# Kernel optimization log

Hardware: AMD Instinct MI355X
Metric: run time of the kernel (lower is better)

Reference implementation:

```python
import jax, jax.numpy as jnp
import numpy as np

WINDOW = 3
RATIO = 5


def _box_filter(x, win):
    """Depthwise 3D box (mean) filter, 'same' padding, per channel.
    x: [N, C, D, H, W] -> [N, C, D, H, W]
    Matches torch conv3d with ones([1,1,w,w,w])/w^3 applied per channel.
    """
    c = x.shape[1]
    k = jnp.ones((c, 1, win, win, win), x.dtype) / (win ** 3)
    pad = win // 2
    return jax.lax.conv_general_dilated(
        x, k,
        window_strides=(1, 1, 1),
        padding=[(pad, pad)] * 3,
        dimension_numbers=('NCDHW', 'OIDHW', 'NCDHW'),
        feature_group_count=c,
    )


def setup_inputs() -> dict:
    key = jax.random.key(0)
    k1, k2 = jax.random.split(key)
    y_pred = jax.random.normal(k1, (1, 3, 192, 192, 192), dtype=jnp.float32)
    y_true = jax.random.uniform(k2, (1, 1, 192, 192, 192), dtype=jnp.float32)
    return {"y_pred": y_pred, "y_true": y_true}


def reference(y_pred, y_true):
    # Finite differences (abs), each [1, 3, D-1, H-1, W-1]
    base = y_pred[:, :, :-1, :-1, :-1]
    dy = jnp.abs(y_pred[:, :, 1:, :-1, :-1] - base)
    dx = jnp.abs(y_pred[:, :, :-1, 1:, :-1] - base)
    dz = jnp.abs(y_pred[:, :, :-1, :-1, 1:] - base)

    # 9 box-filtered single-channel maps == 3 depthwise box filters
    fx = _box_filter(dx, WINDOW)
    fy = _box_filter(dy, WINDOW)
    fz = _box_filter(dz, WINDOW)
    dxdx, dxdy, dxdz = fx[:, 1:2], fy[:, 1:2], fz[:, 1:2]
    dydx, dydy, dydz = fx[:, 0:1], fy[:, 0:1], fz[:, 0:1]
    dzdx, dzdy, dzdz = fx[:, 2:3], fy[:, 2:3], fz[:, 2:3]

    # Neo-Hookean invariants
    det_1 = (dxdx + 1) * ((dydy + 1) * (dzdz + 1) - dydz * dzdy)
    det_2 = -dxdy * (dydx * (dzdz + 1) - dydz * dzdx)
    det_3 = dxdz * (dydx * dzdy - (dydy + 1) * dzdx)
    J = det_1 + det_2 + det_3

    Tr = ((dxdx + 1) ** 2 + dxdy ** 2 + dxdz ** 2
          + dydx ** 2 + (dydy + 1) ** 2 + dydz ** 2
          + dzdx ** 2 + dzdy ** 2 + (dzdz + 1) ** 2)

    # mode == 'exp'
    stretch = Tr * jnp.exp(-J + 1) - 3
    vol_change = (J - 1) ** 2

    # Faithful replication of the sequential mu/lambda normalization in torch:
    mu = 1.0
    lam = mu * RATIO
    mu = mu / (mu + lam)          # 1/6
    lam = lam / (mu + lam)        # 30/31 (uses updated mu, as in source)

    U = mu / 2 * stretch + lam / 2 * vol_change
    return jnp.mean(U)
```

## Files before the change

kernel.cpp:

```cpp
#include <hip/hip_runtime.h>
#include <math.h>

#define DIM 192
#define OD  191
#define PLANE 36864
#define VOL  7077888
#define TH  16
#define TW  16
#define NBH 12
#define CD  14
#define NCH 14

typedef float f4 __attribute__((ext_vector_type(4)));
typedef _Float16 h8 __attribute__((ext_vector_type(8)));
typedef _Float16 h2 __attribute__((ext_vector_type(2)));

__global__ __launch_bounds__(256, 8)
void nh_fused_kernel(const float* __restrict__ P, float* __restrict__ out) {
    const int tid = threadIdx.x;
    const int tx  = tid & 15;
    const int ty  = tid >> 4;
    const int w0  = blockIdx.x * TW;
    const int h0  = blockIdx.y * TH;
    const int ds  = blockIdx.z * CD;
    const int de  = min(ds + CD, OD);

    __shared__ f4 sraw[2][19][20];
    __shared__ h8 sA[18][19];
    __shared__ h2 sB[18][19];
    __shared__ float wsum[4];

    const bool valid = (w0 + tx < OD) && (h0 + ty < OD);

    h8 a0 = (h8)0, a1 = (h8)0, a2 = (h8)0;
    h2 b0 = (h2)0, b1 = (h2)0, b2 = (h2)0;
    float acc = 0.f;

    for (int t = ds - 1; t <= de + 1; ++t) {
        const int cb = t & 1, pb = cb ^ 1;

        if (t >= 0 && t < DIM) {
            for (int l = tid; l < 19 * 19; l += 256) {
                const int hh = l / 19;
                const int ww = l - hh * 19;
                const int hp = h0 - 1 + hh;
                const int wp = w0 - 1 + ww;
                if (hp >= 0 && hp < DIM && wp >= 0 && wp < DIM) {
                    const size_t base = ((size_t)t * DIM + (size_t)hp) * DIM + (size_t)wp;
                    f4 r;
                    r.x = P[base];
                    r.y = P[base + VOL];
                    r.z = P[base + 2 * VOL];
                    r.w = 0.f;
                    sraw[cb][hh][ww] = r;
                }
            }
        }
        __syncthreads();

        const int p = t - 1;
        const bool pplane = (p >= 0) && (p < OD) && (t >= ds);
        for (int l = tid; l < 18 * 18; l += 256) {
            const int hh = l / 18;
            const int ww = l - hh * 18;
            const int hp = h0 - 1 + hh;
            const int wp = w0 - 1 + ww;
            h8 va = (h8)0;
            h2 vb = (h2)0;
            if (pplane && hp >= 0 && hp < OD && wp >= 0 && wp < OD) {
                const f4 c  = sraw[pb][hh][ww];
                const f4 ch = sraw[pb][hh + 1][ww];
                const f4 cw = sraw[pb][hh][ww + 1];
                const f4 cd = sraw[cb][hh][ww];
                const float hx = fabsf(ch.x - c.x), hy = fabsf(ch.y - c.y), hz = fabsf(ch.z - c.z);
                const float dx_ = fabsf(cd.x - c.x), dy_ = fabsf(cd.y - c.y), dz_ = fabsf(cd.z - c.z);
                const float wx = fabsf(cw.x - c.x), wy = fabsf(cw.y - c.y), wz = fabsf(cw.z - c.z);
                va = (h8){(_Float16)hx, (_Float16)hy, (_Float16)hz,
                          (_Float16)dx_, (_Float16)dy_, (_Float16)dz_,
                          (_Float16)wx, (_Float16)wy};
                vb = (h2){(_Float16)wz, (_Float16)0.f};
            }
            sA[hh][ww] = va;
            sB[hh][ww] = vb;
        }
        __syncthreads();

        a0 = a1; a1 = a2; b0 = b1; b1 = b2;
        {
            h8 sa = (h8)0;
            h2 sb = (h2)0;
            #pragma unroll
            for (int j = 0; j < 3; ++j) {
                #pragma unroll
                for (int k = 0; k < 3; ++k) {
                    sa += sA[ty + j][tx + k];
                    sb += sB[ty + j][tx + k];
                }
            }
            a2 = sa; b2 = sb;
        }

        const int d = t - 2;
        if (valid && d >= ds && d < de) {
            const h8 FA = a0 + a1 + a2;
            const h2 FB = b0 + b1 + b2;
            const float inv27 = 1.f / 27.f;
            const float dydx = (float)FA[0] * inv27, dxdx = (float)FA[1] * inv27, dzdx = (float)FA[2] * inv27;
            const float dydy = (float)FA[3] * inv27, dxdy = (float)FA[4] * inv27, dzdy = (float)FA[5] * inv27;
            const float dydz = (float)FA[6] * inv27, dxdz = (float)FA[7] * inv27, dzdz = (float)FB[0] * inv27;
            const float a = dxdx + 1.f, e = dydy + 1.f, iN = dzdz + 1.f;
            const float J = a * (e * iN - dydz * dzdy)
                          - dxdy * (dydx * iN - dydz * dzdx)
                          + dxdz * (dydx * dzdy - e * dzdx);
            const float Tr = a * a + dxdy * dxdy + dxdz * dxdz
                           + dydx * dydx + e * e + dydz * dydz
                           + dzdx * dzdx + dzdy * dzdy + iN * iN;
            const float stretch = Tr * expf(1.f - J) - 3.f;
            const float vol = (J - 1.f) * (J - 1.f);
            acc += 0.0833333358f * stretch + 0.4838709677f * vol;
        }
    }

    acc *= (1.f / 6967871.f);

    #pragma unroll
    for (int off = 32; off > 0; off >>= 1) acc += __shfl_down(acc, off, 64);
    if ((tid & 63) == 0) wsum[tid >> 6] = acc;
    __syncthreads();
    if (tid == 0) {
        atomicAdd(out, wsum[0] + wsum[1] + wsum[2] + wsum[3]);
    }
}

extern "C" void kernel_launch(void* const* d_in, const int* in_sizes, int n_in,
                              void* d_out, int out_size, void* d_ws, size_t ws_size,
                              hipStream_t stream) {
    const float* y_pred = (const float*)d_in[0];
    float* out = (float*)d_out;

    hipMemsetAsync(out, 0, sizeof(float), stream);

    dim3 grid(NBH, NBH, NCH);
    nh_fused_kernel<<<grid, 256, 0, stream>>>(y_pred, out);
}
```

Measured before the change: 190.6 us.

## Use DPP cross-lane W-sums and register-resident center plane to cut LDS traffic

Restructures the tile so each thread owns one loaded voxel kept in registers across planes. The W-direction 3-tap sum now uses DPP row shifts instead of LDS reads, and the output tile narrows to 14 columns so halos fit inside 16-lane rows. Only H-direction sums go through shared memory, and depth chunks grow to 24 planes to reduce halo reloads. The cost is a per-thread register carry, two extra wavefronts handling halo rows, narrower output tiles that waste 2 of 16 lanes, and lower occupancy bounds.

```diff
diff --git a/kernel.cpp b/kernel.cpp
--- a/kernel.cpp
+++ b/kernel.cpp
@@ -3,19 +3,54 @@
 
 #define DIM 192
 #define OD  191
-#define PLANE 36864
-#define VOL  7077888
+#define VOL 7077888
+#define TW  14
 #define TH  16
-#define TW  16
+#define CD  24
+#define NBW 14
 #define NBH 12
-#define CD  14
-#define NCH 14
-
-typedef float f4 __attribute__((ext_vector_type(4)));
+#define NCH 8
+
+typedef float    f4 __attribute__((ext_vector_type(4)));
 typedef _Float16 h8 __attribute__((ext_vector_type(8)));
 typedef _Float16 h2 __attribute__((ext_vector_type(2)));
 
-__global__ __launch_bounds__(256, 8)
+template<int CTRL>
+__device__ __forceinline__ int dppi(int x) {
+    return __builtin_amdgcn_update_dpp(0, x, CTRL, 0xF, 0xF, true);
+}
+
+union U8 { h8 v; int i[4]; };
+union U2 { h2 v; int i; };
+
+__device__ __forceinline__ void wsum3(h8& a, h2& b) {
+    U8 ua, s1, s2;
+    ua.v = a;
+    #pragma unroll
+    for (int k = 0; k < 4; ++k) {
+        s1.i[k] = dppi<0x101>(ua.i[k]);
+        s2.i[k] = dppi<0x111>(ua.i[k]);
+    }
+    a = ua.v + s1.v + s2.v;
+    U2 ub, t1, t2;
+    ub.v = b;
+    t1.i = dppi<0x101>(ub.i);
+    t2.i = dppi<0x111>(ub.i);
+    b = ub.v + t1.v + t2.v;
+}
+
+__device__ __forceinline__ void make_diff(const f4 c, const f4 cw, const f4 ch, const f4 cd,
+                                          h8& va, h2& vb) {
+    const float hx  = fabsf(ch.x - c.x), hy  = fabsf(ch.y - c.y), hz  = fabsf(ch.z - c.z);
+    const float dx_ = fabsf(cd.x - c.x), dy_ = fabsf(cd.y - c.y), dz_ = fabsf(cd.z - c.z);
+    const float wx  = fabsf(cw.x - c.x), wy  = fabsf(cw.y - c.y), wz  = fabsf(cw.z - c.z);
+    va = (h8){(_Float16)hx,  (_Float16)hy,  (_Float16)hz,
+              (_Float16)dx_, (_Float16)dy_, (_Float16)dz_,
+              (_Float16)wx,  (_Float16)wy};
+    vb = (h2){(_Float16)wz, (_Float16)0.f};
+}
+
+__global__ __launch_bounds__(256, 6)
 void nh_fused_kernel(const float* __restrict__ P, float* __restrict__ out) {
     const int tid = threadIdx.x;
     const int tx  = tid & 15;
@@ -25,79 +60,103 @@
     const int ds  = blockIdx.z * CD;
     const int de  = min(ds + CD, OD);
 
-    __shared__ f4 sraw[2][19][20];
-    __shared__ h8 sA[18][19];
-    __shared__ h2 sB[18][19];
+    __shared__ f4 sraw[2][19][18];
+    __shared__ h8 sW[18][16];
+    __shared__ h2 sWB[18][16];
     __shared__ float wsum[4];
 
-    const bool valid = (w0 + tx < OD) && (h0 + ty < OD);
+    const bool valid = (tx < TW) && (w0 + tx < OD) && (h0 + ty < OD);
 
     h8 a0 = (h8)0, a1 = (h8)0, a2 = (h8)0;
     h2 b0 = (h2)0, b1 = (h2)0, b2 = (h2)0;
+    f4 cur = (f4)0, prev = (f4)0;
     float acc = 0.f;
 
     for (int t = ds - 1; t <= de + 1; ++t) {
         const int cb = t & 1, pb = cb ^ 1;
 
         if (t >= 0 && t < DIM) {
-            for (int l = tid; l < 19 * 19; l += 256) {
-                const int hh = l / 19;
-                const int ww = l - hh * 19;
-                const int hp = h0 - 1 + hh;
-                const int wp = w0 - 1 + ww;
+            {
+                const int hp = h0 - 1 + ty;
+                const int wp = w0 - 1 + tx;
+                f4 r = (f4)0;
                 if (hp >= 0 && hp < DIM && wp >= 0 && wp < DIM) {
                     const size_t base = ((size_t)t * DIM + (size_t)hp) * DIM + (size_t)wp;
-                    f4 r;
                     r.x = P[base];
                     r.y = P[base + VOL];
                     r.z = P[base + 2 * VOL];
-                    r.w = 0.f;
-                    sraw[cb][hh][ww] = r;
-                }
-            }
+                }
+                sraw[cb][ty][tx] = r;
+                cur = r;
+            }
+            if (tid < 67) {
+                int hh, ww;
+                if (tid < 16) { hh = tid; ww = 16; }
+                else { const int l = tid - 16; const int q = l / 17; hh = 16 + q; ww = l - 17 * q; }
+                const int hp = h0 - 1 + hh;
+                const int wp = w0 - 1 + ww;
+                f4 r = (f4)0;
+                if (hp >= 0 && hp < DIM && wp >= 0 && wp < DIM) {
+                    const size_t base = ((size_t)t * DIM + (size_t)hp) * DIM + (size_t)wp;
+                    r.x = P[base];
+                    r.y = P[base + VOL];
+                    r.z = P[base + 2 * VOL];
+                }
+                sraw[cb][hh][ww] = r;
+            }
+        } else {
+            cur = (f4)0;
         }
         __syncthreads();
 
         const int p = t - 1;
-        const bool pplane = (p >= 0) && (p < OD) && (t >= ds);
-        for (int l = tid; l < 18 * 18; l += 256) {
-            const int hh = l / 18;
-            const int ww = l - hh * 18;
-            const int hp = h0 - 1 + hh;
-            const int wp = w0 - 1 + ww;
-            h8 va = (h8)0;
-            h2 vb = (h2)0;
-            if (pplane && hp >= 0 && hp < OD && wp >= 0 && wp < OD) {
-                const f4 c  = sraw[pb][hh][ww];
-                const f4 ch = sraw[pb][hh + 1][ww];
-                const f4 cw = sraw[pb][hh][ww + 1];
-                const f4 cd = sraw[cb][hh][ww];
-                const float hx = fabsf(ch.x - c.x), hy = fabsf(ch.y - c.y), hz = fabsf(ch.z - c.z);
-                const float dx_ = fabsf(cd.x - c.x), dy_ = fabsf(cd.y - c.y), dz_ = fabsf(cd.z - c.z);
-                const float wx = fabsf(cw.x - c.x), wy = fabsf(cw.y - c.y), wz = fabsf(cw.z - c.z);
-                va = (h8){(_Float16)hx, (_Float16)hy, (_Float16)hz,
-                          (_Float16)dx_, (_Float16)dy_, (_Float16)dz_,
-                          (_Float16)wx, (_Float16)wy};
-                vb = (h2){(_Float16)wz, (_Float16)0.f};
-            }
-            sA[hh][ww] = va;
-            sB[hh][ww] = vb;
+        const bool built = (p >= 0) && (p < OD) && (t >= ds);
+
+        {
+            h8 sa = (h8)0; h2 sb = (h2)0;
+            if (built) {
+                const int hp = h0 - 1 + ty;
+                const int wp = w0 - 1 + tx;
+                h8 va = (h8)0; h2 vb = (h2)0;
+                if (hp >= 0 && hp < OD && wp >= 0 && wp < OD) {
+                    const f4 c  = prev;
+                    const f4 cw = sraw[pb][ty][tx + 1];
+                    const f4 ch = sraw[pb][ty + 1][tx];
+                    const f4 cd = cur;
+                    make_diff(c, cw, ch, cd, va, vb);
+                }
+                wsum3(va, vb);
+                sa = va; sb = vb;
+            }
+            sW[ty][tx] = sa; sWB[ty][tx] = sb;
+        }
+        if (tid < 32) {
+            const int rr   = 16 + (tid >> 4);
+            const int lane = tid & 15;
+            h8 sa = (h8)0; h2 sb = (h2)0;
+            if (built) {
+                const int hp = h0 - 1 + rr;
+                const int wp = w0 - 1 + lane;
+                h8 va = (h8)0; h2 vb = (h2)0;
+                if (hp >= 0 && hp < OD && wp >= 0 && wp < OD) {
+                    const f4 c  = sraw[pb][rr][lane];
+                    const f4 cw = sraw[pb][rr][lane + 1];
+                    const f4 ch = sraw[pb][rr + 1][lane];
+                    const f4 cd = sraw[cb][rr][lane];
+                    make_diff(c, cw, ch, cd, va, vb);
+                }
+                wsum3(va, vb);
+                sa = va; sb = vb;
+            }
+            sW[rr][lane] = sa; sWB[rr][lane] = sb;
         }
         __syncthreads();
 
         a0 = a1; a1 = a2; b0 = b1; b1 = b2;
         {
-            h8 sa = (h8)0;
-            h2 sb = (h2)0;
-            #pragma unroll
-            for (int j = 0; j < 3; ++j) {
-                #pragma unroll
-                for (int k = 0; k < 3; ++k) {
-                    sa += sA[ty + j][tx + k];
-                    sb += sB[ty + j][tx + k];
-                }
-            }
-            a2 = sa; b2 = sb;
+            const int cc = (tx + 1) & 15;
+            a2 = sW[ty][cc] + sW[ty + 1][cc] + sW[ty + 2][cc];
+            b2 = sWB[ty][cc] + sWB[ty + 1][cc] + sWB[ty + 2][cc];
         }
 
         const int d = t - 2;
@@ -119,6 +178,8 @@
             const float vol = (J - 1.f) * (J - 1.f);
             acc += 0.0833333358f * stretch + 0.4838709677f * vol;
         }
+
+        prev = cur;
     }
 
     acc *= (1.f / 6967871.f);
@@ -140,6 +201,6 @@
 
     hipMemsetAsync(out, 0, sizeof(float), stream);
 
-    dim3 grid(NBH, NBH, NCH);
+    dim3 grid(NBW, NBH, NCH);
     nh_fused_kernel<<<grid, 256, 0, stream>>>(y_pred, out);
 }
```

Result: faster. 183.6 us (-3.6%).
